# Optimization experiments

Hardware: AMD Instinct MI355X
Metric: run time of the kernel (lower is better)

Reference implementation:

```python
import jax, jax.numpy as jnp
from jax import lax
import numpy as np

T, B, D, H, L, HO, OUT = 256, 4096, 32, 256, 32, 512, 8
DELTA = 1.0  # delta_next


def setup_inputs() -> dict:
    key = jax.random.key(0)
    ks = jax.random.split(key, 20)
    g = lambda i, shape, s: jax.random.normal(ks[i], shape, jnp.float32) * s
    x_history = jax.random.normal(ks[0], (T, B, D), jnp.float32)
    # strictly increasing times, identical across batch (as in a shared grid)
    t_history = jnp.broadcast_to((jnp.arange(T, dtype=jnp.float32) * 0.1)[:, None, None], (T, B, 1))
    inp = {
        "x_history": x_history,
        "t_history": t_history,
        # GRU (PyTorch gate order r,z,n), stored as (in, 3H)
        "W_ih": g(1, (D + 1, 3 * H), 0.05), "W_hh": g(2, (H, 3 * H), 0.05),
        "b_ih": jnp.zeros((3 * H,), jnp.float32), "b_hh": jnp.zeros((3 * H,), jnp.float32),
        # hid2lat
        "W_lat": g(3, (H, 2 * L), 0.05), "b_lat": jnp.zeros((2 * L,), jnp.float32),
        # ODE func 3-layer tanh MLP (xavier gain 0.1 in original -> small init)
        "W1": g(4, (L, HO), 0.02), "b1": jnp.zeros((HO,), jnp.float32),
        "W2": g(5, (HO, HO), 0.02), "b2": jnp.zeros((HO,), jnp.float32),
        "W3": g(6, (HO, L), 0.02), "b3": jnp.zeros((L,), jnp.float32),
        # decoder
        "Wd1": g(7, (L, H), 0.05), "bd1": jnp.zeros((H,), jnp.float32),
        "Wd2": g(8, (H, OUT), 0.05), "bd2": jnp.zeros((OUT,), jnp.float32),
    }
    return inp


def reference(x_history, t_history, W_ih, W_hh, b_ih, b_hh, W_lat, b_lat,
              W1, b1, W2, b2, W3, b3, Wd1, bd1, Wd2, bd2):
    latent = b_lat.shape[0] // 2
    # dt: dt[0]=0, dt[i]=t[i]-t[i-1]
    dt = jnp.concatenate([jnp.zeros_like(t_history[:1]), t_history[1:] - t_history[:-1]], axis=0)
    xt = jnp.concatenate([x_history, dt], axis=-1)          # [T, B, D+1]
    seq = xt[::-1]                                           # GRU over flipped sequence

    def gru_step(h, x_t):
        gi = x_t @ W_ih + b_ih                               # [B, 3H]
        gh = h @ W_hh + b_hh
        i_r, i_z, i_n = jnp.split(gi, 3, axis=-1)
        h_r, h_z, h_n = jnp.split(gh, 3, axis=-1)
        r = jax.nn.sigmoid(i_r + h_r)
        z = jax.nn.sigmoid(i_z + h_z)
        n = jnp.tanh(i_n + r * h_n)
        return (1.0 - z) * n + z * h, None

    h0 = jnp.zeros((x_history.shape[1], W_hh.shape[0]), x_history.dtype)
    hT, _ = lax.scan(gru_step, h0, seq)
    z0 = (hT @ W_lat + b_lat)[:, :latent]                    # z_mean, [B, L]

    def f(z):  # ODE func: 3-layer tanh MLP, t-independent
        return jnp.tanh(jnp.tanh(z @ W1 + b1) @ W2 + b2) @ W3 + b3

    # torchdiffeq 'rk4' = single 3/8-rule step over [t0, t0+DELTA]
    hstep = jnp.asarray(DELTA, z0.dtype)
    k1 = f(z0)
    k2 = f(z0 + hstep * k1 / 3.0)
    k3 = f(z0 + hstep * (k2 - k1 / 3.0))
    k4 = f(z0 + hstep * (k1 - k2 + k3))
    zT = z0 + hstep * (k1 + 3.0 * k2 + 3.0 * k3 + k4) / 8.0

    return jax.nn.relu(zT @ Wd1 + bd1) @ Wd2 + bd2           # [B, OUT]
```

## Files before the change

### kernel.cpp

```cpp
#include <hip/hip_runtime.h>

typedef _Float16 f16;
typedef _Float16 h8 __attribute__((ext_vector_type(8)));
typedef float f32x4 __attribute__((ext_vector_type(4)));

#define MFMA16(a,b,c) __builtin_amdgcn_mfma_f32_16x16x32_f16((a),(b),(c),0,0,0)
#define MFMA8(a,b,c)  __builtin_amdgcn_mfma_f32_16x16x32_fp8_bf8((long)(a),(long)(b),(c),0,0,0)

#define TT 256
#define BB 4096
#define OUTD 8

#define WS_WHH    0u
#define WS_WIHHI  393216u
#define WS_WIHLO  442368u
#define WS_WLON   466944u
#define WS_WLAT   532480u
#define WS_W1T    548864u
#define WS_W2T    581632u
#define WS_W3T    1105920u
#define WS_WD1T   1138688u
#define WS_WD2T   1155072u

#define L_HB     0
#define L_WRT    16384
#define L_CST    147456
#define LDS_SIZE 155648

__device__ __forceinline__ float fsigm(float x) {
  return __builtin_amdgcn_rcpf(1.f + __builtin_amdgcn_exp2f(-1.44269504f * x));
}
__device__ __forceinline__ float ftanh(float x) {
  return 1.f - 2.f * __builtin_amdgcn_rcpf(1.f + __builtin_amdgcn_exp2f(2.88539008f * x));
}
__device__ __forceinline__ f32x4 splat4(float v) { f32x4 r = {v, v, v, v}; return r; }

__device__ __forceinline__ long long pack_e4m3_h8(h8 a) {
  int lo = __builtin_amdgcn_cvt_pk_fp8_f32((float)a[0], (float)a[1], 0, false);
  lo = __builtin_amdgcn_cvt_pk_fp8_f32((float)a[2], (float)a[3], lo, true);
  int hi = __builtin_amdgcn_cvt_pk_fp8_f32((float)a[4], (float)a[5], 0, false);
  hi = __builtin_amdgcn_cvt_pk_fp8_f32((float)a[6], (float)a[7], hi, true);
  return (long long)(unsigned)lo | ((long long)hi << 32);
}
__device__ __forceinline__ long long pack_e4m3_f32x8(f32x4 a, f32x4 b) {
  int lo = __builtin_amdgcn_cvt_pk_fp8_f32(a[0], a[1], 0, false);
  lo = __builtin_amdgcn_cvt_pk_fp8_f32(a[2], a[3], lo, true);
  int hi = __builtin_amdgcn_cvt_pk_fp8_f32(b[0], b[1], 0, false);
  hi = __builtin_amdgcn_cvt_pk_fp8_f32(b[2], b[3], hi, true);
  return (long long)(unsigned)lo | ((long long)hi << 32);
}

__global__ __launch_bounds__(512) void prep_kernel(
    const float* __restrict__ Wih, const float* __restrict__ Whh,
    const float* __restrict__ Wlat, const float* __restrict__ W1,
    const float* __restrict__ W2, const float* __restrict__ W3,
    const float* __restrict__ Wd1, const float* __restrict__ Wd2,
    char* __restrict__ ws) {
  int idx = blockIdx.x * 512 + threadIdx.x;
  if (idx < 768*256) {
    int n = idx >> 8, k = idx & 255;
    ((f16*)(ws + WS_WHH))[n*256 + k] = (f16)(Whh[k*768 + n] * 256.f);
  }
  if (idx < 768*32) {
    int n = idx >> 5, k = idx & 31;
    ((f16*)(ws + WS_WIHHI))[n*32 + k] = (f16)(Wih[k*768 + n] * 256.f);
  }
  if (idx < 768*16) {
    int n = idx >> 4, k2 = (idx & 15) * 2;
    float w0 = Wih[k2*768 + n] * 256.f;
    float w1 = Wih[(k2+1)*768 + n] * 256.f;
    float r0 = w0 - (float)(f16)w0;
    float r1 = w1 - (float)(f16)w1;
    int p = __builtin_amdgcn_cvt_pk_bf8_f32(r0, r1, 0, false);
    *(short*)(ws + WS_WIHLO + n*32 + k2) = (short)p;
  }
  if (idx < 256*128) {
    int n = idx >> 7, k2 = (idx & 127) * 2;
    int c = 512 + n;
    float w0 = Whh[k2*768 + c] * 256.f;
    float w1 = Whh[(k2+1)*768 + c] * 256.f;
    float r0 = w0 - (float)(f16)w0;
    float r1 = w1 - (float)(f16)w1;
    int p = __builtin_amdgcn_cvt_pk_bf8_f32(r0, r1, 0, false);
    *(short*)(ws + WS_WLON + n*256 + k2) = (short)p;
  }
  if (idx < 32*256)  { int n = idx >> 8, k = idx & 255; ((f16*)(ws + WS_WLAT))[n*256 + k] = (f16)Wlat[k*64 + n]; }
  if (idx < 512*32)  { int n = idx >> 5, k = idx & 31;  ((f16*)(ws + WS_W1T))[n*32 + k]   = (f16)W1[k*512 + n]; }
  if (idx < 512*512) { int n = idx >> 9, k = idx & 511; ((f16*)(ws + WS_W2T))[n*512 + k]  = (f16)W2[k*512 + n]; }
  if (idx < 32*512)  { int n = idx >> 9, k = idx & 511; ((f16*)(ws + WS_W3T))[n*512 + k]  = (f16)W3[k*32 + n]; }
  if (idx < 256*32)  { int n = idx >> 5, k = idx & 31;  ((f16*)(ws + WS_WD1T))[n*32 + k]  = (f16)Wd1[k*256 + n]; }
  if (idx < 16*256)  { int n = idx >> 8, k = idx & 255; ((f16*)(ws + WS_WD2T))[n*256 + k] = (n < 8) ? (f16)Wd2[k*8 + n] : (f16)0.f; }
}

__global__ __launch_bounds__(512) __attribute__((amdgpu_waves_per_eu(2, 2)))
void gru_ode_kernel(
    const float* __restrict__ xh, const float* __restrict__ th,
    const float* __restrict__ Wih_f, const float* __restrict__ bih,
    const float* __restrict__ bhh, const float* __restrict__ blat,
    const float* __restrict__ b1, const float* __restrict__ b2,
    const float* __restrict__ b3, const float* __restrict__ bd1,
    const float* __restrict__ bd2, const char* __restrict__ ws,
    float* __restrict__ out) {
  extern __shared__ char smem[];
  char* HB  = smem + L_HB;
  char* WRT = smem + L_WRT;
  float* CST = (float*)(smem + L_CST);
  const char* wlng = ws + WS_WLON;
  const char* wilg = ws + WS_WIHLO;
  const char* wihg = ws + WS_WIHHI;

  const int tid  = threadIdx.x;
  const int wave = tid >> 6;
  const int lane = tid & 63;
  const int lq   = lane >> 4;
  const int lr   = lane & 15;
  const int m0   = blockIdx.x << 4;
  const int swz  = (lr & 7) << 4;
  const int lq16 = lq * 16, lq8 = lq * 8;
  const float S  = 1.f / 256.f;

  #pragma unroll
  for (int it = 0; it < 8; ++it) ((unsigned*)HB)[tid + it*512] = 0u;
  {
    #pragma unroll
    for (int it = 0; it < 64; ++it) {
      int i = tid + it*512;
      int row = i >> 7, kw = i & 127;
      unsigned v = *(const unsigned*)(ws + WS_WHH + row*512 + kw*4);
      *(unsigned*)(WRT + row*512 + ((kw*4) ^ ((row & 7) << 4))) = v;
    }
  }
  if (tid < 256) {
    int c = tid;
    CST[c*7 + 0] = Wih_f[32*768 + c];
    CST[c*7 + 1] = Wih_f[32*768 + 256 + c];
    CST[c*7 + 2] = Wih_f[32*768 + 512 + c];
    CST[c*7 + 3] = bih[c] + bhh[c];
    CST[c*7 + 4] = bih[256 + c] + bhh[256 + c];
    CST[c*7 + 5] = bih[512 + c];
    CST[c*7 + 6] = bhh[512 + c];
  }

  h8 Wfz[2][8], Wfn[2][8];
  #pragma unroll
  for (int t = 0; t < 2; ++t) {
    const char* bz = ws + WS_WHH + (256 + wave*32 + t*16 + lr)*512 + lq16;
    const char* bn = ws + WS_WHH + (512 + wave*32 + t*16 + lr)*512 + lq16;
    #pragma unroll
    for (int kc = 0; kc < 8; ++kc) {
      Wfz[t][kc] = *(const h8*)(bz + kc*64);
      Wfn[t][kc] = *(const h8*)(bn + kc*64);
    }
  }

  float hreg[2][4];
  #pragma unroll
  for (int t = 0; t < 2; ++t)
    #pragma unroll
    for (int r = 0; r < 4; ++r) hreg[t][r] = 0.f;

  const int wrt0 = (wave*32 + lr)*512;
  const int wln0 = (wave*32 + lr)*256;

  __syncthreads();

  #pragma unroll 1
  for (int s = 0; s < 256; ++s) {
    const int tsrc = 255 - s;
    f32x4 xa = *(const f32x4*)(xh + (size_t)(tsrc*BB + m0 + lr)*32 + lq8);
    f32x4 xb = *(const f32x4*)(xh + (size_t)(tsrc*BB + m0 + lr)*32 + lq8 + 4);
    f32x4 tha = *(const f32x4*)(th + tsrc*BB + m0 + lq*4);
    f32x4 thb = tha;
    if (tsrc > 0) thb = *(const f32x4*)(th + (tsrc-1)*BB + m0 + lq*4);

    f32x4 accR[2], accZ[2], accNH[2], accNI[2];
    #pragma unroll
    for (int t = 0; t < 2; ++t) { accR[t] = splat4(0.f); accZ[t] = splat4(0.f); accNH[t] = splat4(0.f); accNI[t] = splat4(0.f); }

    #pragma unroll
    for (int kc = 0; kc < 8; ++kc) {
      const int ko = (kc*64 + lq16) ^ swz;
      h8 ahi = *(const h8*)(HB + lr*1024 + ko);
      h8 alo = *(const h8*)(HB + lr*1024 + 512 + ko);
      h8 wr0 = *(const h8*)(WRT + wrt0 + ko);
      h8 wr1 = *(const h8*)(WRT + wrt0 + 8192 + ko);
      accR[0] = MFMA16(ahi, wr0, accR[0]);       accR[0] = MFMA16(alo, wr0, accR[0]);
      accR[1] = MFMA16(ahi, wr1, accR[1]);       accR[1] = MFMA16(alo, wr1, accR[1]);
      accZ[0] = MFMA16(ahi, Wfz[0][kc], accZ[0]); accZ[0] = MFMA16(alo, Wfz[0][kc], accZ[0]);
      accZ[1] = MFMA16(ahi, Wfz[1][kc], accZ[1]); accZ[1] = MFMA16(alo, Wfz[1][kc], accZ[1]);
      accNH[0] = MFMA16(ahi, Wfn[0][kc], accNH[0]); accNH[0] = MFMA16(alo, Wfn[0][kc], accNH[0]);
      accNH[1] = MFMA16(ahi, Wfn[1][kc], accNH[1]); accNH[1] = MFMA16(alo, Wfn[1][kc], accNH[1]);
      long long a8 = pack_e4m3_h8(ahi);
      long long b80 = *(const long long*)(wlng + wln0 + kc*32 + lq8);
      long long b81 = *(const long long*)(wlng + wln0 + 4096 + kc*32 + lq8);
      accNH[0] = MFMA8(a8, b80, accNH[0]);
      accNH[1] = MFMA8(a8, b81, accNH[1]);
    }

    h8 xhi, xlo;
    #pragma unroll
    for (int j = 0; j < 8; ++j) {
      float v = (j < 4) ? xa[j] : xb[j-4];
      f16 h = (f16)v;
      xhi[j] = h; xlo[j] = (f16)(v - (float)h);
    }
    long long ax8 = pack_e4m3_f32x8(xa, xb);
    #pragma unroll
    for (int t = 0; t < 2; ++t) {
      int nr =       wave*32 + t*16 + lr;
      int nz = 256 + wave*32 + t*16 + lr;
      int nn = 512 + wave*32 + t*16 + lr;
      h8 br_ = *(const h8*)(wihg + nr*64 + lq16);
      h8 bz_ = *(const h8*)(wihg + nz*64 + lq16);
      h8 bn_ = *(const h8*)(wihg + nn*64 + lq16);
      accR[t]  = MFMA16(xhi, br_, accR[t]);  accR[t]  = MFMA16(xlo, br_, accR[t]);
      accZ[t]  = MFMA16(xhi, bz_, accZ[t]);  accZ[t]  = MFMA16(xlo, bz_, accZ[t]);
      accNI[t] = MFMA16(xhi, bn_, accNI[t]); accNI[t] = MFMA16(xlo, bn_, accNI[t]);
      long long br8 = *(const long long*)(wilg + nr*32 + lq8);
      long long bz8 = *(const long long*)(wilg + nz*32 + lq8);
      long long bn8 = *(const long long*)(wilg + nn*32 + lq8);
      accR[t]  = MFMA8(ax8, br8, accR[t]);
      accZ[t]  = MFMA8(ax8, bz8, accZ[t]);
      accNI[t] = MFMA8(ax8, bn8, accNI[t]);
    }

    __syncthreads();

    float dtv[4];
    #pragma unroll
    for (int r = 0; r < 4; ++r) dtv[r] = tha[r] - thb[r];
    #pragma unroll
    for (int t = 0; t < 2; ++t) {
      int c = wave*32 + t*16 + lr;
      const float* cc = CST + c*7;
      float w32r = cc[0], w32z = cc[1], w32n = cc[2];
      float br = cc[3], bz = cc[4], bin = cc[5], bhn = cc[6];
      #pragma unroll
      for (int r = 0; r < 4; ++r) {
        float rv = accR[t][r]*S + br + dtv[r]*w32r;
        float zv = accZ[t][r]*S + bz + dtv[r]*w32z;
        float iv = accNI[t][r]*S + bin + dtv[r]*w32n;
        float hn = accNH[t][r]*S + bhn;
        float rg = fsigm(rv), zg = fsigm(zv);
        float nv = ftanh(iv + rg*hn);
        float hv = nv + zg*(hreg[t][r] - nv);
        hreg[t][r] = hv;
        int row = lq*4 + r;
        f16 hh = (f16)hv;
        *(f16*)(HB + row*1024 + ((2*c) ^ ((row & 7) << 4))) = hh;
        *(f16*)(HB + row*1024 + 512 + ((2*c) ^ ((row & 7) << 4))) = (f16)(hv - (float)hh);
      }
    }
    __syncthreads();
  }

  f32x4 z0a = splat4(blat[lr]);
  f32x4 z0b = splat4(blat[16 + lr]);
  #pragma unroll
  for (int kc = 0; kc < 8; ++kc) {
    h8 ahi = *(const h8*)(HB + lr*1024 + ((kc*64 + lq16) ^ swz));
    h8 alo = *(const h8*)(HB + lr*1024 + 512 + ((kc*64 + lq16) ^ swz));
    h8 ba = *(const h8*)(ws + WS_WLAT + lr*512 + kc*64 + lq16);
    h8 bb = *(const h8*)(ws + WS_WLAT + (16 + lr)*512 + kc*64 + lq16);
    z0a = MFMA16(ahi, ba, z0a); z0a = MFMA16(alo, ba, z0a);
    z0b = MFMA16(ahi, bb, z0b); z0b = MFMA16(alo, bb, z0b);
  }

  char* TZ  = smem + L_WRT;
  char* TU1 = smem + L_WRT + 2048;
  char* TU2 = smem + L_WRT + 18432;
  char* TD  = smem + L_WRT + 34816;

  auto Ffun = [&](f32x4 zina, f32x4 zinb, f32x4& ka, f32x4& kb) {
    if (wave == 0) {
      #pragma unroll
      for (int r = 0; r < 4; ++r) {
        int row = lq*4 + r;
        *(f16*)(TZ + row*64 + ((2*lr) ^ ((row & 3) << 4))) = (f16)zina[r];
        *(f16*)(TZ + row*64 + ((2*(16 + lr)) ^ ((row & 3) << 4))) = (f16)zinb[r];
      }
    }
    __syncthreads();
    h8 za = *(const h8*)(TZ + lr*64 + ((lq16) ^ ((lr & 3) << 4)));
    #pragma unroll
    for (int st = 0; st < 4; ++st) {
      int n = wave*64 + st*16 + lr;
      f32x4 t0 = splat4(b1[n]);
      t0 = MFMA16(za, *(const h8*)(ws + WS_W1T + n*64 + lq16), t0);
      #pragma unroll
      for (int r = 0; r < 4; ++r) {
        int row = lq*4 + r;
        *(f16*)(TU1 + row*1024 + ((2*n) ^ ((row & 7) << 4))) = (f16)ftanh(t0[r]);
      }
    }
    __syncthreads();
    #pragma unroll
    for (int st = 0; st < 4; ++st) {
      int n = wave*64 + st*16 + lr;
      f32x4 t0 = splat4(b2[n]);
      #pragma unroll
      for (int kc = 0; kc < 16; ++kc) {
        h8 a = *(const h8*)(TU1 + lr*1024 + ((kc*64 + lq16) ^ ((lr & 7) << 4)));
        t0 = MFMA16(a, *(const h8*)(ws + WS_W2T + n*1024 + kc*64 + lq16), t0);
      }
      #pragma unroll
      for (int r = 0; r < 4; ++r) {
        int row = lq*4 + r;
        *(f16*)(TU2 + row*1024 + ((2*n) ^ ((row & 7) << 4))) = (f16)ftanh(t0[r]);
      }
    }
    __syncthreads();
    f32x4 t0 = splat4(b3[lr]), t1 = splat4(b3[16 + lr]);
    #pragma unroll
    for (int kc = 0; kc < 16; ++kc) {
      h8 a = *(const h8*)(TU2 + lr*1024 + ((kc*64 + lq16) ^ ((lr & 7) << 4)));
      t0 = MFMA16(a, *(const h8*)(ws + WS_W3T + lr*1024 + kc*64 + lq16), t0);
      t1 = MFMA16(a, *(const h8*)(ws + WS_W3T + (16 + lr)*1024 + kc*64 + lq16), t1);
    }
    ka = t0; kb = t1;
    __syncthreads();
  };

  f32x4 k1a, k1b, k2a, k2b, k3a, k3b, k4a, k4b;
  Ffun(z0a, z0b, k1a, k1b);
  Ffun(z0a + k1a*(1.f/3.f), z0b + k1b*(1.f/3.f), k2a, k2b);
  Ffun(z0a + k2a - k1a*(1.f/3.f), z0b + k2b - k1b*(1.f/3.f), k3a, k3b);
  Ffun(z0a + k1a - k2a + k3a, z0b + k1b - k2b + k3b, k4a, k4b);
  f32x4 zTa = z0a + (k1a + 3.f*k2a + 3.f*k3a + k4a)*0.125f;
  f32x4 zTb = z0b + (k1b + 3.f*k2b + 3.f*k3b + k4b)*0.125f;

  if (wave == 0) {
    #pragma unroll
    for (int r = 0; r < 4; ++r) {
      int row = lq*4 + r;
      *(f16*)(TZ + row*64 + ((2*lr) ^ ((row & 3) << 4))) = (f16)zTa[r];
      *(f16*)(TZ + row*64 + ((2*(16 + lr)) ^ ((row & 3) << 4))) = (f16)zTb[r];
    }
  }
  __syncthreads();
  {
    h8 za = *(const h8*)(TZ + lr*64 + ((lq16) ^ ((lr & 3) << 4)));
    #pragma unroll
    for (int st = 0; st < 2; ++st) {
      int n = wave*32 + st*16 + lr;
      f32x4 t0 = splat4(bd1[n]);
      t0 = MFMA16(za, *(const h8*)(ws + WS_WD1T + n*64 + lq16), t0);
      #pragma unroll
      for (int r = 0; r < 4; ++r) {
        int row = lq*4 + r;
        float v = t0[r] > 0.f ? t0[r] : 0.f;
        *(f16*)(TD + row*512 + ((2*n) ^ ((row & 7) << 4))) = (f16)v;
      }
    }
  }
  __syncthreads();
  if (wave == 0) {
    f32x4 o = splat4(0.f);
    #pragma unroll
    for (int kc = 0; kc < 8; ++kc) {
      h8 a = *(const h8*)(TD + lr*512 + ((kc*64 + lq16) ^ ((lr & 7) << 4)));
      o = MFMA16(a, *(const h8*)(ws + WS_WD2T + lr*512 + kc*64 + lq16), o);
    }
    if (lr < OUTD) {
      float q = bd2[lr];
      #pragma unroll
      for (int r = 0; r < 4; ++r) out[(m0 + lq*4 + r)*OUTD + lr] = o[r] + q;
    }
  }
}

extern "C" void kernel_launch(void* const* d_in, const int* in_sizes, int n_in,
                              void* d_out, int out_size, void* d_ws, size_t ws_size,
                              hipStream_t stream) {
  const float* x    = (const float*)d_in[0];
  const float* th   = (const float*)d_in[1];
  const float* Wih  = (const float*)d_in[2];
  const float* Whh  = (const float*)d_in[3];
  const float* bih  = (const float*)d_in[4];
  const float* bhh  = (const float*)d_in[5];
  const float* Wlat = (const float*)d_in[6];
  const float* blat = (const float*)d_in[7];
  const float* W1   = (const float*)d_in[8];
  const float* b1   = (const float*)d_in[9];
  const float* W2   = (const float*)d_in[10];
  const float* b2   = (const float*)d_in[11];
  const float* W3   = (const float*)d_in[12];
  const float* b3   = (const float*)d_in[13];
  const float* Wd1  = (const float*)d_in[14];
  const float* bd1  = (const float*)d_in[15];
  const float* Wd2  = (const float*)d_in[16];
  const float* bd2  = (const float*)d_in[17];
  (void)in_sizes; (void)n_in; (void)out_size; (void)ws_size;

  static int lds_set = 0;
  if (!lds_set) {
    hipFuncSetAttribute((const void*)gru_ode_kernel,
                        hipFuncAttributeMaxDynamicSharedMemorySize, LDS_SIZE);
    lds_set = 1;
  }

  prep_kernel<<<512, 512, 0, stream>>>(Wih, Whh, Wlat, W1, W2, W3, Wd1, Wd2, (char*)d_ws);
  gru_ode_kernel<<<256, 512, LDS_SIZE, stream>>>(x, th, Wih, bih, bhh, blat, b1, b2, b3,
                                                 bd1, bd2, (const char*)d_ws, (float*)d_out);
}
```

Baseline: 2.561 ms.

## Halve block to 4 waves, stash recurrent weights in AGPRs

Shrinks the GRU kernel from 8 waves to 4 waves per block, so each wave now computes 64 hidden columns instead of 32. Most of the z and n recurrent weight fragments are written into accumulation registers with inline asm and read back each step. The remaining n-gate slice stays in ordinary VGPRs, and the r-gate weights still come from LDS. This keeps more weights in registers and spreads the per-step sync and overhead over more work per wave. The cost is fewer waves available to hide latency, extra accvgpr read instructions, and a longer serial chain of MFMAs per wave.

```diff
diff --git a/kernel.cpp b/kernel.cpp
--- a/kernel.cpp
+++ b/kernel.cpp
@@ -27,6 +27,23 @@
 #define L_CST    147456
 #define LDS_SIZE 155648
 
+#define DECLW(p) int p##_0, p##_1, p##_2, p##_3
+#define STASH(p, addr) do { \
+  union { h8 h; int i[4]; } u_; u_.h = *(const h8*)(addr); \
+  asm volatile("v_accvgpr_write_b32 %0, %1" : "=a"(p##_0) : "v"(u_.i[0])); \
+  asm volatile("v_accvgpr_write_b32 %0, %1" : "=a"(p##_1) : "v"(u_.i[1])); \
+  asm volatile("v_accvgpr_write_b32 %0, %1" : "=a"(p##_2) : "v"(u_.i[2])); \
+  asm volatile("v_accvgpr_write_b32 %0, %1" : "=a"(p##_3) : "v"(u_.i[3])); \
+} while (0)
+#define AREAD(dst, p) do { \
+  union { h8 h; int i[4]; } u_; \
+  asm volatile("v_accvgpr_read_b32 %0, %1" : "=v"(u_.i[0]) : "a"(p##_0)); \
+  asm volatile("v_accvgpr_read_b32 %0, %1" : "=v"(u_.i[1]) : "a"(p##_1)); \
+  asm volatile("v_accvgpr_read_b32 %0, %1" : "=v"(u_.i[2]) : "a"(p##_2)); \
+  asm volatile("v_accvgpr_read_b32 %0, %1" : "=v"(u_.i[3]) : "a"(p##_3)); \
+  dst = u_.h; \
+} while (0)
+
 __device__ __forceinline__ float fsigm(float x) {
   return __builtin_amdgcn_rcpf(1.f + __builtin_amdgcn_exp2f(-1.44269504f * x));
 }
@@ -92,7 +109,7 @@
   if (idx < 16*256)  { int n = idx >> 8, k = idx & 255; ((f16*)(ws + WS_WD2T))[n*256 + k] = (n < 8) ? (f16)Wd2[k*8 + n] : (f16)0.f; }
 }
 
-__global__ __launch_bounds__(512) __attribute__((amdgpu_waves_per_eu(2, 2)))
+__global__ __launch_bounds__(256, 1) __attribute__((amdgpu_waves_per_eu(1, 1)))
 void gru_ode_kernel(
     const float* __restrict__ xh, const float* __restrict__ th,
     const float* __restrict__ Wih_f, const float* __restrict__ bih,
@@ -120,17 +137,16 @@
   const float S  = 1.f / 256.f;
 
   #pragma unroll
-  for (int it = 0; it < 8; ++it) ((unsigned*)HB)[tid + it*512] = 0u;
+  for (int it = 0; it < 16; ++it) ((unsigned*)HB)[tid + it*256] = 0u;
   {
-    #pragma unroll
-    for (int it = 0; it < 64; ++it) {
-      int i = tid + it*512;
+    for (int it = 0; it < 128; ++it) {
+      int i = tid + it*256;
       int row = i >> 7, kw = i & 127;
       unsigned v = *(const unsigned*)(ws + WS_WHH + row*512 + kw*4);
       *(unsigned*)(WRT + row*512 + ((kw*4) ^ ((row & 7) << 4))) = v;
     }
   }
-  if (tid < 256) {
+  {
     int c = tid;
     CST[c*7 + 0] = Wih_f[32*768 + c];
     CST[c*7 + 1] = Wih_f[32*768 + 256 + c];
@@ -141,26 +157,51 @@
     CST[c*7 + 6] = bhh[512 + c];
   }
 
-  h8 Wfz[2][8], Wfn[2][8];
+  DECLW(Z00); DECLW(Z01); DECLW(Z02); DECLW(Z03); DECLW(Z04); DECLW(Z05); DECLW(Z06); DECLW(Z07);
+  DECLW(Z10); DECLW(Z11); DECLW(Z12); DECLW(Z13); DECLW(Z14); DECLW(Z15); DECLW(Z16); DECLW(Z17);
+  DECLW(Z20); DECLW(Z21); DECLW(Z22); DECLW(Z23); DECLW(Z24); DECLW(Z25); DECLW(Z26); DECLW(Z27);
+  DECLW(Z30); DECLW(Z31); DECLW(Z32); DECLW(Z33); DECLW(Z34); DECLW(Z35); DECLW(Z36); DECLW(Z37);
+  DECLW(N00); DECLW(N01); DECLW(N02); DECLW(N03); DECLW(N04); DECLW(N05); DECLW(N06); DECLW(N07);
+  DECLW(N10); DECLW(N11); DECLW(N12); DECLW(N13); DECLW(N14); DECLW(N15); DECLW(N16); DECLW(N17);
+  DECLW(N20); DECLW(N21); DECLW(N22); DECLW(N23); DECLW(N24); DECLW(N25); DECLW(N26); DECLW(N27);
+  {
+    const char* bz0 = ws + WS_WHH + (256 + wave*64 + 0*16 + lr)*512 + lq16;
+    const char* bz1 = ws + WS_WHH + (256 + wave*64 + 1*16 + lr)*512 + lq16;
+    const char* bz2 = ws + WS_WHH + (256 + wave*64 + 2*16 + lr)*512 + lq16;
+    const char* bz3 = ws + WS_WHH + (256 + wave*64 + 3*16 + lr)*512 + lq16;
+    const char* bn0 = ws + WS_WHH + (512 + wave*64 + 0*16 + lr)*512 + lq16;
+    const char* bn1 = ws + WS_WHH + (512 + wave*64 + 1*16 + lr)*512 + lq16;
+    const char* bn2 = ws + WS_WHH + (512 + wave*64 + 2*16 + lr)*512 + lq16;
+    STASH(Z00, bz0+0); STASH(Z01, bz0+64); STASH(Z02, bz0+128); STASH(Z03, bz0+192);
+    STASH(Z04, bz0+256); STASH(Z05, bz0+320); STASH(Z06, bz0+384); STASH(Z07, bz0+448);
+    STASH(Z10, bz1+0); STASH(Z11, bz1+64); STASH(Z12, bz1+128); STASH(Z13, bz1+192);
+    STASH(Z14, bz1+256); STASH(Z15, bz1+320); STASH(Z16, bz1+384); STASH(Z17, bz1+448);
+    STASH(Z20, bz2+0); STASH(Z21, bz2+64); STASH(Z22, bz2+128); STASH(Z23, bz2+192);
+    STASH(Z24, bz2+256); STASH(Z25, bz2+320); STASH(Z26, bz2+384); STASH(Z27, bz2+448);
+    STASH(Z30, bz3+0); STASH(Z31, bz3+64); STASH(Z32, bz3+128); STASH(Z33, bz3+192);
+    STASH(Z34, bz3+256); STASH(Z35, bz3+320); STASH(Z36, bz3+384); STASH(Z37, bz3+448);
+    STASH(N00, bn0+0); STASH(N01, bn0+64); STASH(N02, bn0+128); STASH(N03, bn0+192);
+    STASH(N04, bn0+256); STASH(N05, bn0+320); STASH(N06, bn0+384); STASH(N07, bn0+448);
+    STASH(N10, bn1+0); STASH(N11, bn1+64); STASH(N12, bn1+128); STASH(N13, bn1+192);
+    STASH(N14, bn1+256); STASH(N15, bn1+320); STASH(N16, bn1+384); STASH(N17, bn1+448);
+    STASH(N20, bn2+0); STASH(N21, bn2+64); STASH(N22, bn2+128); STASH(N23, bn2+192);
+    STASH(N24, bn2+256); STASH(N25, bn2+320); STASH(N26, bn2+384); STASH(N27, bn2+448);
+  }
+  h8 Wn3[8];
+  {
+    const char* bn3 = ws + WS_WHH + (512 + wave*64 + 3*16 + lr)*512 + lq16;
+    #pragma unroll
+    for (int kc = 0; kc < 8; ++kc) Wn3[kc] = *(const h8*)(bn3 + kc*64);
+  }
+
+  float hreg[4][4];
   #pragma unroll
-  for (int t = 0; t < 2; ++t) {
-    const char* bz = ws + WS_WHH + (256 + wave*32 + t*16 + lr)*512 + lq16;
-    const char* bn = ws + WS_WHH + (512 + wave*32 + t*16 + lr)*512 + lq16;
-    #pragma unroll
-    for (int kc = 0; kc < 8; ++kc) {
-      Wfz[t][kc] = *(const h8*)(bz + kc*64);
-      Wfn[t][kc] = *(const h8*)(bn + kc*64);
-    }
-  }
-
-  float hreg[2][4];
-  #pragma unroll
-  for (int t = 0; t < 2; ++t)
+  for (int t = 0; t < 4; ++t)
     #pragma unroll
     for (int r = 0; r < 4; ++r) hreg[t][r] = 0.f;
 
-  const int wrt0 = (wave*32 + lr)*512;
-  const int wln0 = (wave*32 + lr)*256;
+  const int wrtb = (wave*64 + lr)*512;
+  const int wlnb = (wave*64 + lr)*256;
 
   __syncthreads();
 
@@ -173,29 +214,39 @@
     f32x4 thb = tha;
     if (tsrc > 0) thb = *(const f32x4*)(th + (tsrc-1)*BB + m0 + lq*4);
 
-    f32x4 accR[2], accZ[2], accNH[2], accNI[2];
-    #pragma unroll
-    for (int t = 0; t < 2; ++t) { accR[t] = splat4(0.f); accZ[t] = splat4(0.f); accNH[t] = splat4(0.f); accNI[t] = splat4(0.f); }
-
-    #pragma unroll
-    for (int kc = 0; kc < 8; ++kc) {
-      const int ko = (kc*64 + lq16) ^ swz;
-      h8 ahi = *(const h8*)(HB + lr*1024 + ko);
-      h8 alo = *(const h8*)(HB + lr*1024 + 512 + ko);
-      h8 wr0 = *(const h8*)(WRT + wrt0 + ko);
-      h8 wr1 = *(const h8*)(WRT + wrt0 + 8192 + ko);
-      accR[0] = MFMA16(ahi, wr0, accR[0]);       accR[0] = MFMA16(alo, wr0, accR[0]);
-      accR[1] = MFMA16(ahi, wr1, accR[1]);       accR[1] = MFMA16(alo, wr1, accR[1]);
-      accZ[0] = MFMA16(ahi, Wfz[0][kc], accZ[0]); accZ[0] = MFMA16(alo, Wfz[0][kc], accZ[0]);
-      accZ[1] = MFMA16(ahi, Wfz[1][kc], accZ[1]); accZ[1] = MFMA16(alo, Wfz[1][kc], accZ[1]);
-      accNH[0] = MFMA16(ahi, Wfn[0][kc], accNH[0]); accNH[0] = MFMA16(alo, Wfn[0][kc], accNH[0]);
-      accNH[1] = MFMA16(ahi, Wfn[1][kc], accNH[1]); accNH[1] = MFMA16(alo, Wfn[1][kc], accNH[1]);
-      long long a8 = pack_e4m3_h8(ahi);
-      long long b80 = *(const long long*)(wlng + wln0 + kc*32 + lq8);
-      long long b81 = *(const long long*)(wlng + wln0 + 4096 + kc*32 + lq8);
-      accNH[0] = MFMA8(a8, b80, accNH[0]);
-      accNH[1] = MFMA8(a8, b81, accNH[1]);
-    }
+    f32x4 accR[4], accZ[4], accNH[4], accNI[4];
+    #pragma unroll
+    for (int t = 0; t < 4; ++t) { accR[t] = splat4(0.f); accZ[t] = splat4(0.f); accNH[t] = splat4(0.f); accNI[t] = splat4(0.f); }
+
+#define HP(k) { \
+    const int ko = ((k)*64 + lq16) ^ swz; \
+    h8 ahi = *(const h8*)(HB + lr*1024 + ko); \
+    h8 alo = *(const h8*)(HB + lr*1024 + 512 + ko); \
+    h8 wr0 = *(const h8*)(WRT + wrtb + 0*8192 + ko); \
+    h8 wr1 = *(const h8*)(WRT + wrtb + 1*8192 + ko); \
+    h8 wr2 = *(const h8*)(WRT + wrtb + 2*8192 + ko); \
+    h8 wr3 = *(const h8*)(WRT + wrtb + 3*8192 + ko); \
+    accR[0] = MFMA16(ahi, wr0, accR[0]); accR[0] = MFMA16(alo, wr0, accR[0]); \
+    accR[1] = MFMA16(ahi, wr1, accR[1]); accR[1] = MFMA16(alo, wr1, accR[1]); \
+    accR[2] = MFMA16(ahi, wr2, accR[2]); accR[2] = MFMA16(alo, wr2, accR[2]); \
+    accR[3] = MFMA16(ahi, wr3, accR[3]); accR[3] = MFMA16(alo, wr3, accR[3]); \
+    h8 wz; \
+    AREAD(wz, Z0##k); accZ[0] = MFMA16(ahi, wz, accZ[0]); accZ[0] = MFMA16(alo, wz, accZ[0]); \
+    AREAD(wz, Z1##k); accZ[1] = MFMA16(ahi, wz, accZ[1]); accZ[1] = MFMA16(alo, wz, accZ[1]); \
+    AREAD(wz, Z2##k); accZ[2] = MFMA16(ahi, wz, accZ[2]); accZ[2] = MFMA16(alo, wz, accZ[2]); \
+    AREAD(wz, Z3##k); accZ[3] = MFMA16(ahi, wz, accZ[3]); accZ[3] = MFMA16(alo, wz, accZ[3]); \
+    AREAD(wz, N0##k); accNH[0] = MFMA16(ahi, wz, accNH[0]); accNH[0] = MFMA16(alo, wz, accNH[0]); \
+    AREAD(wz, N1##k); accNH[1] = MFMA16(ahi, wz, accNH[1]); accNH[1] = MFMA16(alo, wz, accNH[1]); \
+    AREAD(wz, N2##k); accNH[2] = MFMA16(ahi, wz, accNH[2]); accNH[2] = MFMA16(alo, wz, accNH[2]); \
+    accNH[3] = MFMA16(ahi, Wn3[k], accNH[3]); accNH[3] = MFMA16(alo, Wn3[k], accNH[3]); \
+    long long a8 = pack_e4m3_h8(ahi); \
+    accNH[0] = MFMA8(a8, *(const long long*)(wlng + wlnb + 0*4096 + (k)*32 + lq8), accNH[0]); \
+    accNH[1] = MFMA8(a8, *(const long long*)(wlng + wlnb + 1*4096 + (k)*32 + lq8), accNH[1]); \
+    accNH[2] = MFMA8(a8, *(const long long*)(wlng + wlnb + 2*4096 + (k)*32 + lq8), accNH[2]); \
+    accNH[3] = MFMA8(a8, *(const long long*)(wlng + wlnb + 3*4096 + (k)*32 + lq8), accNH[3]); \
+  }
+    HP(0) HP(1) HP(2) HP(3) HP(4) HP(5) HP(6) HP(7)
+#undef HP
 
     h8 xhi, xlo;
     #pragma unroll
@@ -206,10 +257,10 @@
     }
     long long ax8 = pack_e4m3_f32x8(xa, xb);
     #pragma unroll
-    for (int t = 0; t < 2; ++t) {
-      int nr =       wave*32 + t*16 + lr;
-      int nz = 256 + wave*32 + t*16 + lr;
-      int nn = 512 + wave*32 + t*16 + lr;
+    for (int t = 0; t < 4; ++t) {
+      int nr =       wave*64 + t*16 + lr;
+      int nz = 256 + wave*64 + t*16 + lr;
+      int nn = 512 + wave*64 + t*16 + lr;
       h8 br_ = *(const h8*)(wihg + nr*64 + lq16);
       h8 bz_ = *(const h8*)(wihg + nz*64 + lq16);
       h8 bn_ = *(const h8*)(wihg + nn*64 + lq16);
@@ -230,8 +281,8 @@
     #pragma unroll
     for (int r = 0; r < 4; ++r) dtv[r] = tha[r] - thb[r];
     #pragma unroll
-    for (int t = 0; t < 2; ++t) {
-      int c = wave*32 + t*16 + lr;
+    for (int t = 0; t < 4; ++t) {
+      int c = wave*64 + t*16 + lr;
       const float* cc = CST + c*7;
       float w32r = cc[0], w32z = cc[1], w32n = cc[2];
       float br = cc[3], bz = cc[4], bin = cc[5], bhn = cc[6];
@@ -283,8 +334,8 @@
     __syncthreads();
     h8 za = *(const h8*)(TZ + lr*64 + ((lq16) ^ ((lr & 3) << 4)));
     #pragma unroll
-    for (int st = 0; st < 4; ++st) {
-      int n = wave*64 + st*16 + lr;
+    for (int st = 0; st < 8; ++st) {
+      int n = wave*128 + st*16 + lr;
       f32x4 t0 = splat4(b1[n]);
       t0 = MFMA16(za, *(const h8*)(ws + WS_W1T + n*64 + lq16), t0);
       #pragma unroll
@@ -295,8 +346,8 @@
     }
     __syncthreads();
     #pragma unroll
-    for (int st = 0; st < 4; ++st) {
-      int n = wave*64 + st*16 + lr;
+    for (int st = 0; st < 8; ++st) {
+      int n = wave*128 + st*16 + lr;
       f32x4 t0 = splat4(b2[n]);
       #pragma unroll
       for (int kc = 0; kc < 16; ++kc) {
@@ -341,8 +392,8 @@
   {
     h8 za = *(const h8*)(TZ + lr*64 + ((lq16) ^ ((lr & 3) << 4)));
     #pragma unroll
-    for (int st = 0; st < 2; ++st) {
-      int n = wave*32 + st*16 + lr;
+    for (int st = 0; st < 4; ++st) {
+      int n = wave*64 + st*16 + lr;
       f32x4 t0 = splat4(bd1[n]);
       t0 = MFMA16(za, *(const h8*)(ws + WS_WD1T + n*64 + lq16), t0);
       #pragma unroll
@@ -400,6 +451,6 @@
   }
 
   prep_kernel<<<512, 512, 0, stream>>>(Wih, Whh, Wlat, W1, W2, W3, Wd1, Wd2, (char*)d_ws);
-  gru_ode_kernel<<<256, 512, LDS_SIZE, stream>>>(x, th, Wih, bih, bhh, blat, b1, b2, b3,
+  gru_ode_kernel<<<256, 256, LDS_SIZE, stream>>>(x, th, Wih, bih, bhh, blat, b1, b2, b3,
                                                  bd1, bd2, (const char*)d_ws, (float*)d_out);
 }
```

Measured after the change: 3.244 ms. 1.27x slower.
